# Optimization experiments

Hardware: AMD Instinct MI355X
Metric: run time of the kernel (lower is better)

## Reference

```python
import jax, jax.numpy as jnp
import numpy as np

D_MODEL = 256
D_INNER = 512   # expand * dim
D_STATE = 16
D_CONV = 4
DT_RANK = 16    # ceil(dim / 16)
PATCH = 64


def _silu(v):
    return v * jax.nn.sigmoid(v)


def _causal_dwconv(x, w, b):
    # x: (b, d, l); w: (d, 1, k) depthwise; causal left pad k-1
    y = jax.lax.conv_general_dilated(
        x, w, window_strides=(1,), padding=[(D_CONV - 1, 0)],
        feature_group_count=D_INNER, dimension_numbers=("NCH", "OIH", "NCH"))
    return y + b[None, :, None]


def _selective_scan(u, delta, A, Bm, Cm, Dp):
    # u, delta: (b, d, l); A: (d, n); Bm, Cm: (b, n, l)
    dA = jnp.exp(jnp.einsum("bdl,dn->lbdn", delta, A))
    dBu = jnp.einsum("bdl,bnl,bdl->lbdn", delta, Bm, u)
    Ct = jnp.transpose(Cm, (2, 0, 1))  # (l, b, n)

    def step(h, inp):
        dA_t, dBu_t, c_t = inp
        h = dA_t * h + dBu_t
        return h, jnp.einsum("bdn,bn->bd", h, c_t)

    h0 = jnp.zeros(u.shape[:2] + (A.shape[1],), u.dtype)
    _, ys = jax.lax.scan(step, h0, (dA, dBu, Ct))  # ys: (l, b, d)
    return jnp.transpose(ys, (1, 2, 0)) + Dp[None, :, None] * u


def _mamba_branch(xz, conv_w, conv_b, xproj_w, dtp_w, dtp_b, A_log, Dp):
    xpart, z = jnp.split(xz, 2, axis=1)  # each (b, d_inner, l)
    xc = _silu(_causal_dwconv(xpart, conv_w, conv_b))
    xdbl = jnp.einsum("bdl,ed->bel", xc, xproj_w)  # e = dt_rank + 2*d_state
    dt = xdbl[:, :DT_RANK]
    Bm = xdbl[:, DT_RANK:DT_RANK + D_STATE]
    Cm = xdbl[:, DT_RANK + D_STATE:]
    delta = jax.nn.softplus(jnp.einsum("brl,dr->bdl", dt, dtp_w) + dtp_b[None, :, None])
    A = -jnp.exp(A_log)
    y = _selective_scan(xc, delta, A, Bm, Cm, Dp)
    return y * _silu(z)


def setup_inputs():
    key = jax.random.key(0)
    ks = jax.random.split(key, 16)

    def nrm(k, shape, s=0.02):
        return jax.random.normal(k, shape, jnp.float32) * s

    A_init = jnp.log(jnp.tile(jnp.arange(1, D_STATE + 1, dtype=jnp.float32), (D_INNER, 1)))
    return {
        "x": jax.random.normal(ks[0], (2, D_MODEL, 4096), jnp.float32),
        "ln_g": jnp.ones((D_MODEL,), jnp.float32),
        "ln_b": jnp.zeros((D_MODEL,), jnp.float32),
        "in_proj_w": nrm(ks[1], (2 * D_INNER, D_MODEL)),
        "conv_w": nrm(ks[2], (D_INNER, 1, D_CONV), 0.1),
        "conv_b": nrm(ks[3], (D_INNER,), 0.01),
        "x_proj_w": nrm(ks[4], (DT_RANK + 2 * D_STATE, D_INNER)),
        "dt_proj_w": nrm(ks[5], (D_INNER, DT_RANK), 0.1),
        "dt_proj_b": nrm(ks[6], (D_INNER,), 0.1),
        "A_log": A_init,
        "D_f": jnp.ones((D_INNER,), jnp.float32),
        "conv_w_b": nrm(ks[7], (D_INNER, 1, D_CONV), 0.1),
        "conv_b_b": nrm(ks[8], (D_INNER,), 0.01),
        "x_proj_w_b": nrm(ks[9], (DT_RANK + 2 * D_STATE, D_INNER)),
        "dt_proj_w_b": nrm(ks[10], (D_INNER, DT_RANK), 0.1),
        "dt_proj_b_b": nrm(ks[11], (D_INNER,), 0.1),
        "A_b_log": A_init,
        "D_b": jnp.ones((D_INNER,), jnp.float32),
        "out_proj_w": nrm(ks[12], (D_MODEL, D_INNER)),
        "depth": 4,
    }


def reference(x, ln_g, ln_b, in_proj_w, conv_w, conv_b, x_proj_w, dt_proj_w,
              dt_proj_b, A_log, D_f, conv_w_b, conv_b_b, x_proj_w_b,
              dt_proj_w_b, dt_proj_b_b, A_b_log, D_b, out_proj_w, depth):
    assert depth in (3, 4, 5)
    B, C, L = x.shape
    ps = PATCH
    xp, Lp = x, L
    if L % ps != 0:  # borrow-pad (static shape logic, mirrors torch code)
        pad_len = ps - L % ps
        start = max(L - L % ps - pad_len, 0)
        xp = jnp.concatenate([x, x[:, :, start:start + pad_len]], axis=2)
        Lp = L + pad_len
    npt = Lp // ps
    # (B, C, npt, ps) -> (B*ps, C, npt) -> (B*ps, npt, C)
    xd = xp.reshape(B, C, npt, ps).transpose(0, 3, 1, 2).reshape(B * ps, C, npt)
    xf = jnp.transpose(xd, (0, 2, 1))
    # LayerNorm over channel dim
    mu = xf.mean(-1, keepdims=True)
    var = ((xf - mu) ** 2).mean(-1, keepdims=True)
    xn = (xf - mu) * jax.lax.rsqrt(var + 1e-5) * ln_g + ln_b
    # in_proj -> (b, 2*d_inner, l)
    xz = jnp.einsum("blc,ec->bel", xn, in_proj_w)
    y_f = _mamba_branch(xz, conv_w, conv_b, x_proj_w, dt_proj_w, dt_proj_b, A_log, D_f)
    y_b = _mamba_branch(xz[:, :, ::-1], conv_w_b, conv_b_b, x_proj_w_b,
                        dt_proj_w_b, dt_proj_b_b, A_b_log, D_b)[:, :, ::-1]
    y = y_f + y_b
    out_m = jnp.einsum("bdl,cd->blc", y, out_proj_w)  # (B*ps, npt, C)
    # mirrors torch: reshape(B, ps, npt, C).permute(0,3,1,2).reshape(B, C, Lp)
    xo = out_m.reshape(B, ps, npt, C).transpose(0, 3, 1, 2).reshape(B, C, Lp)
    xo = xo[:, :, :L]
    return xo + x
```

## Files before the change

kernel.cpp:

```cpp
#include <hip/hip_runtime.h>


#define OFF_XZ 0
#define OFF_XC 8388608
#define OFF_DL 12582912
#define OFF_BC 16777216
#define OFF_YF 17039360
#define OFF_YB 19136512
#define OFF_WOB 21233664
#define OFF_WX 21299200

typedef __attribute__((ext_vector_type(8))) short short8;
typedef __attribute__((ext_vector_type(4))) float f32x4;

__device__ __forceinline__ float siluf(float v) {
    return v / (1.f + __expf(-v));
}
__device__ __forceinline__ float softplusf(float v) {
    return (v > 20.f) ? v : log1pf(__expf(v));
}
__device__ __forceinline__ unsigned short f2bf(float f) {
    union { float f; unsigned int u; } v; v.f = f;
    unsigned int u = v.u;
    return (unsigned short)((u + 0x7FFFu + ((u >> 16) & 1u)) >> 16);
}

__global__ __launch_bounds__(256) void k_cvt_w(
    const float* __restrict__ W, unsigned short* __restrict__ Wb, int n4)
{
    int i = blockIdx.x * 256 + threadIdx.x;
    if (i >= n4) return;
    float4 v = *(const float4*)(W + i * 4);
    ushort4 o;
    o.x = f2bf(v.x); o.y = f2bf(v.y); o.z = f2bf(v.z); o.w = f2bf(v.w);
    *(ushort4*)(Wb + i * 4) = o;
}

__global__ __launch_bounds__(256) void k_mk_wx(
    const float* __restrict__ W6, const float* __restrict__ dtw,
    unsigned short* __restrict__ Wx)
{
    const int n = blockIdx.x;
    const int c = threadIdx.x;
    if (n < 512) {
        float a0 = 0.f, a1 = 0.f;
        #pragma unroll
        for (int r = 0; r < 16; ++r) {
            float w = dtw[n * 16 + r];
            a0 = fmaf(w, W6[r * 512 + c], a0);
            a1 = fmaf(w, W6[r * 512 + c + 256], a1);
        }
        Wx[n * 512 + c] = f2bf(a0);
        Wx[n * 512 + c + 256] = f2bf(a1);
    } else {
        int rr = n - 496;
        Wx[n * 512 + c] = f2bf(W6[rr * 512 + c]);
        Wx[n * 512 + c + 256] = f2bf(W6[rr * 512 + c + 256]);
    }
}

__global__ __launch_bounds__(256) void k_ln_inproj_mfma(
    const float* __restrict__ x, const float* __restrict__ g,
    const float* __restrict__ bt, const unsigned short* __restrict__ Wb,
    float* __restrict__ xz)
{
    __shared__ unsigned short sxb[64 * 256];
    const int bid = blockIdx.x;
    const int pg = bid >> 2, og = bid & 3;
    const int p0 = pg * 64;
    const int tid = threadIdx.x;
    const int wave = tid >> 6, lane = tid & 63;
    const int b = pg >> 6, pp = pg & 63;
    const float* xb = x + ((size_t)b * 256) * 4096 + pp;

    const int c = lane * 4;
    const float g0 = g[c + 0], g1 = g[c + 1], g2 = g[c + 2], g3 = g[c + 3];
    const float b0 = bt[c + 0], b1 = bt[c + 1], b2 = bt[c + 2], b3 = bt[c + 3];
    for (int i = 0; i < 16; ++i) {
        int m = wave * 16 + i;
        const float* xr = xb + m * 64;
        float v0 = xr[(size_t)(c + 0) * 4096];
        float v1 = xr[(size_t)(c + 1) * 4096];
        float v2 = xr[(size_t)(c + 2) * 4096];
        float v3 = xr[(size_t)(c + 3) * 4096];
        float s = v0 + v1 + v2 + v3;
        #pragma unroll
        for (int o = 32; o; o >>= 1) s += __shfl_xor(s, o);
        float mu = s * (1.f / 256.f);
        float q0 = v0 - mu, q1 = v1 - mu, q2 = v2 - mu, q3 = v3 - mu;
        float q = q0 * q0 + q1 * q1 + q2 * q2 + q3 * q3;
        #pragma unroll
        for (int o = 32; o; o >>= 1) q += __shfl_xor(q, o);
        float rs = rsqrtf(q * (1.f / 256.f) + 1e-5f);
        ushort4 pk;
        pk.x = f2bf(q0 * rs * g0 + b0);
        pk.y = f2bf(q1 * rs * g1 + b1);
        pk.z = f2bf(q2 * rs * g2 + b2);
        pk.w = f2bf(q3 * rs * g3 + b3);
        int byte = m * 512 + lane * 8;
        byte ^= (m & 7) << 4;
        *(ushort4*)((char*)sxb + byte) = pk;
    }
    __syncthreads();

    const int nbase = og * 256 + wave * 64;
    const int l15 = lane & 15, lg = lane >> 4;
    f32x4 acc[4][4];
    #pragma unroll
    for (int mi = 0; mi < 4; ++mi)
        #pragma unroll
        for (int ni = 0; ni < 4; ++ni) acc[mi][ni] = (f32x4){0.f, 0.f, 0.f, 0.f};

    const unsigned short* wrow[4];
    #pragma unroll
    for (int ni = 0; ni < 4; ++ni)
        wrow[ni] = Wb + (size_t)(nbase + ni * 16 + l15) * 256 + lg * 8;

    #pragma unroll 2
    for (int k0 = 0; k0 < 256; k0 += 32) {
        short8 a[4], bfr[4];
        #pragma unroll
        for (int mi = 0; mi < 4; ++mi) {
            int row = mi * 16 + l15;
            int byte = row * 512 + k0 * 2 + lg * 16;
            byte ^= (row & 7) << 4;
            a[mi] = *(const short8*)((const char*)sxb + byte);
        }
        #pragma unroll
        for (int ni = 0; ni < 4; ++ni)
            bfr[ni] = *(const short8*)(wrow[ni] + k0);
        #pragma unroll
        for (int mi = 0; mi < 4; ++mi)
            #pragma unroll
            for (int ni = 0; ni < 4; ++ni)
                acc[mi][ni] = __builtin_amdgcn_mfma_f32_16x16x32_bf16(
                    a[mi], bfr[ni], acc[mi][ni], 0, 0, 0);
    }

    #pragma unroll
    for (int mi = 0; mi < 4; ++mi)
        #pragma unroll
        for (int ni = 0; ni < 4; ++ni)
            #pragma unroll
            for (int r = 0; r < 4; ++r)
                xz[(size_t)(p0 + mi * 16 + lg * 4 + r) * 1024 + nbase + ni * 16 + l15] =
                    acc[mi][ni][r];
}

__global__ __launch_bounds__(256) void k_cxg(
    const float* __restrict__ xz, const float* __restrict__ cw,
    const float* __restrict__ cb, const unsigned short* __restrict__ Wx,
    const float* __restrict__ dtb,
    float* __restrict__ xc, float* __restrict__ delta,
    float* __restrict__ bcb, int rev)
{
    __shared__ unsigned short sxb[64 * 512];
    const int blk = blockIdx.x;
    const int bp = blk >> 1, og = blk & 1;
    const int tid = threadIdx.x;
    const int wave = tid >> 6, lane = tid & 63;
    const size_t xzrow = (size_t)bp * 64;
    const int m0 = wave * 16;

    {
        const int da = lane * 4, db = 256 + lane * 4;
        float4 wa0 = *(const float4*)&cw[(da + 0) * 4];
        float4 wa1 = *(const float4*)&cw[(da + 1) * 4];
        float4 wa2 = *(const float4*)&cw[(da + 2) * 4];
        float4 wa3 = *(const float4*)&cw[(da + 3) * 4];
        float4 wb0 = *(const float4*)&cw[(db + 0) * 4];
        float4 wb1 = *(const float4*)&cw[(db + 1) * 4];
        float4 wb2 = *(const float4*)&cw[(db + 2) * 4];
        float4 wb3 = *(const float4*)&cw[(db + 3) * 4];
        float4 ba = *(const float4*)&cb[da];
        float4 bb = *(const float4*)&cb[db];

        float4 a1 = {0,0,0,0}, a2 = {0,0,0,0}, a3 = {0,0,0,0};
        float4 c1 = {0,0,0,0}, c2 = {0,0,0,0}, c3 = {0,0,0,0};
        if (m0 > 0) {
            int i1 = m0 - 1, i2 = m0 - 2, i3 = m0 - 3;
            int l1 = rev ? 63 - i1 : i1, l2 = rev ? 63 - i2 : i2, l3 = rev ? 63 - i3 : i3;
            a1 = *(const float4*)&xz[(xzrow + l1) * 1024 + da];
            a2 = *(const float4*)&xz[(xzrow + l2) * 1024 + da];
            a3 = *(const float4*)&xz[(xzrow + l3) * 1024 + da];
            c1 = *(const float4*)&xz[(xzrow + l1) * 1024 + db];
            c2 = *(const float4*)&xz[(xzrow + l2) * 1024 + db];
            c3 = *(const float4*)&xz[(xzrow + l3) * 1024 + db];
        }
        for (int p = 0; p < 16; ++p) {
            int i = m0 + p;
            int l = rev ? 63 - i : i;
            float4 cura = *(const float4*)&xz[(xzrow + l) * 1024 + da];
            float4 curb = *(const float4*)&xz[(xzrow + l) * 1024 + db];
            float4 sa, sb;
            sa.x = siluf(wa0.w * cura.x + wa0.z * a1.x + wa0.y * a2.x + wa0.x * a3.x + ba.x);
            sa.y = siluf(wa1.w * cura.y + wa1.z * a1.y + wa1.y * a2.y + wa1.x * a3.y + ba.y);
            sa.z = siluf(wa2.w * cura.z + wa2.z * a1.z + wa2.y * a2.z + wa2.x * a3.z + ba.z);
            sa.w = siluf(wa3.w * cura.w + wa3.z * a1.w + wa3.y * a2.w + wa3.x * a3.w + ba.w);
            sb.x = siluf(wb0.w * curb.x + wb0.z * c1.x + wb0.y * c2.x + wb0.x * c3.x + bb.x);
            sb.y = siluf(wb1.w * curb.y + wb1.z * c1.y + wb1.y * c2.y + wb1.x * c3.y + bb.y);
            sb.z = siluf(wb2.w * curb.z + wb2.z * c1.z + wb2.y * c2.z + wb2.x * c3.z + bb.z);
            sb.w = siluf(wb3.w * curb.w + wb3.z * c1.w + wb3.y * c2.w + wb3.x * c3.w + bb.w);
            if (og == 0) {
                *(float4*)&xc[(xzrow + i) * 512 + da] = sa;
                *(float4*)&xc[(xzrow + i) * 512 + db] = sb;
            }
            ushort4 pa, pb;
            pa.x = f2bf(sa.x); pa.y = f2bf(sa.y); pa.z = f2bf(sa.z); pa.w = f2bf(sa.w);
            pb.x = f2bf(sb.x); pb.y = f2bf(sb.y); pb.z = f2bf(sb.z); pb.w = f2bf(sb.w);
            int bytea = i * 1024 + da * 2; bytea ^= (i & 7) << 4;
            int byteb = i * 1024 + db * 2; byteb ^= (i & 7) << 4;
            *(ushort4*)((char*)sxb + bytea) = pa;
            *(ushort4*)((char*)sxb + byteb) = pb;
            a3 = a2; a2 = a1; a1 = cura;
            c3 = c2; c2 = c1; c1 = curb;
        }
    }
    __syncthreads();

    const int l15 = lane & 15, lg = lane >> 4;
    f32x4 acc[17];
    #pragma unroll
    for (int ni = 0; ni < 17; ++ni) acc[ni] = (f32x4){0.f, 0.f, 0.f, 0.f};
    const unsigned short* bbase = Wx + (size_t)(og * 272 + l15) * 512 + lg * 8;
    const int arow = m0 + l15;
    const int abase = arow * 1024 + lg * 16;
    const int aswz = (arow & 7) << 4;

    for (int k0 = 0; k0 < 512; k0 += 32) {
        short8 af = *(const short8*)((const char*)sxb + ((abase + k0 * 2) ^ aswz));
        #pragma unroll
        for (int ni = 0; ni < 17; ++ni) {
            short8 bw = *(const short8*)(bbase + (size_t)ni * 8192 + k0);
            acc[ni] = __builtin_amdgcn_mfma_f32_16x16x32_bf16(af, bw, acc[ni], 0, 0, 0);
        }
    }

    #pragma unroll
    for (int ni = 0; ni < 17; ++ni) {
        int col = og * 272 + ni * 16 + l15;
        if (col < 512) {
            float bias = dtb[col];
            #pragma unroll
            for (int r = 0; r < 4; ++r) {
                int pos = m0 + lg * 4 + r;
                delta[(xzrow + pos) * 512 + col] = softplusf(acc[ni][r] + bias);
            }
        } else {
            #pragma unroll
            for (int r = 0; r < 4; ++r) {
                int pos = m0 + lg * 4 + r;
                bcb[(xzrow + pos) * 32 + (col - 512)] = acc[ni][r];
            }
        }
    }
}

__global__ __launch_bounds__(256) void k_scan(
    const float* __restrict__ delta, const float* __restrict__ u_,
    const float* __restrict__ bc_, const float* __restrict__ xz,
    const float* __restrict__ A_log, const float* __restrict__ Dp,
    unsigned short* __restrict__ yout, int rev)
{
    const int bid = blockIdx.x;
    const int bp  = bid >> 1;
    const int d   = ((bid & 1) << 8) + threadIdx.x;

    float a[16];
    #pragma unroll
    for (int n = 0; n < 16; ++n) a[n] = -__expf(A_log[(size_t)d * 16 + n]);
    const float Dd = Dp[d];

    float h[16];
    #pragma unroll
    for (int n = 0; n < 16; ++n) h[n] = 0.f;

    for (int l = 0; l < 64; ++l) {
        size_t base = (size_t)bp * 64 + l;
        float dl = delta[base * 512 + d];
        float uu = u_[base * 512 + d];
        float du = dl * uu;
        const float4* bc = (const float4*)(bc_ + base * 32);
        float y = 0.f;
        #pragma unroll
        for (int n4 = 0; n4 < 4; ++n4) {
            float4 Bv = bc[n4];
            float4 Cv = bc[4 + n4];
            int n = n4 * 4;
            h[n + 0] = fmaf(__expf(dl * a[n + 0]), h[n + 0], du * Bv.x); y = fmaf(h[n + 0], Cv.x, y);
            h[n + 1] = fmaf(__expf(dl * a[n + 1]), h[n + 1], du * Bv.y); y = fmaf(h[n + 1], Cv.y, y);
            h[n + 2] = fmaf(__expf(dl * a[n + 2]), h[n + 2], du * Bv.z); y = fmaf(h[n + 2], Cv.z, y);
            h[n + 3] = fmaf(__expf(dl * a[n + 3]), h[n + 3], du * Bv.w); y = fmaf(h[n + 3], Cv.w, y);
        }
        y = fmaf(Dd, uu, y);
        int lo = rev ? 63 - l : l;
        float zv = xz[((size_t)bp * 64 + lo) * 1024 + 512 + d];
        yout[((size_t)bp * 64 + lo) * 512 + d] = f2bf(y * siluf(zv));
    }
}

__global__ __launch_bounds__(256) void k_outproj_mfma(
    const unsigned short* __restrict__ yf, const unsigned short* __restrict__ yb,
    const unsigned short* __restrict__ wob, const float* __restrict__ x,
    float* __restrict__ out)
{
    __shared__ float sD[64][257];
    const int blk = blockIdx.x;
    const int g = blk >> 6, l = blk & 63;
    const int tid = threadIdx.x;
    const int wave = tid >> 6, lane = tid & 63;
    const int l15 = lane & 15, lg = lane >> 4;
    const int cbase = wave * 64;

    f32x4 acc[4][4];
    #pragma unroll
    for (int mi = 0; mi < 4; ++mi)
        #pragma unroll
        for (int ni = 0; ni < 4; ++ni) acc[mi][ni] = (f32x4){0.f, 0.f, 0.f, 0.f};

    const unsigned short* arf[4];
    const unsigned short* arb[4];
    #pragma unroll
    for (int mi = 0; mi < 4; ++mi) {
        size_t idx = (((size_t)(g * 64 + mi * 16 + l15)) * 64 + l) * 512 + lg * 8;
        arf[mi] = yf + idx;
        arb[mi] = yb + idx;
    }
    const unsigned short* brow[4];
    #pragma unroll
    for (int ni = 0; ni < 4; ++ni)
        brow[ni] = wob + (size_t)(cbase + ni * 16 + l15) * 512 + lg * 8;

    #pragma unroll 2
    for (int k0 = 0; k0 < 512; k0 += 32) {
        short8 bw[4], af[4], ab[4];
        #pragma unroll
        for (int ni = 0; ni < 4; ++ni) bw[ni] = *(const short8*)(brow[ni] + k0);
        #pragma unroll
        for (int mi = 0; mi < 4; ++mi) {
            af[mi] = *(const short8*)(arf[mi] + k0);
            ab[mi] = *(const short8*)(arb[mi] + k0);
        }
        #pragma unroll
        for (int mi = 0; mi < 4; ++mi)
            #pragma unroll
            for (int ni = 0; ni < 4; ++ni) {
                acc[mi][ni] = __builtin_amdgcn_mfma_f32_16x16x32_bf16(
                    af[mi], bw[ni], acc[mi][ni], 0, 0, 0);
                acc[mi][ni] = __builtin_amdgcn_mfma_f32_16x16x32_bf16(
                    ab[mi], bw[ni], acc[mi][ni], 0, 0, 0);
            }
    }

    #pragma unroll
    for (int mi = 0; mi < 4; ++mi)
        #pragma unroll
        for (int ni = 0; ni < 4; ++ni)
            #pragma unroll
            for (int r = 0; r < 4; ++r)
                sD[mi * 16 + lg * 4 + r][cbase + ni * 16 + l15] = acc[mi][ni][r];
    __syncthreads();

    #pragma unroll
    for (int q = 0; q < 16; ++q) {
        int f4 = q * 256 + tid;
        int cc = f4 >> 4, m4 = f4 & 15;
        size_t idx = ((size_t)(g * 256 + cc)) * 4096 + (size_t)l * 64 + m4 * 4;
        float4 xr = *(const float4*)(x + idx);
        float4 v;
        v.x = sD[m4 * 4 + 0][cc] + xr.x;
        v.y = sD[m4 * 4 + 1][cc] + xr.y;
        v.z = sD[m4 * 4 + 2][cc] + xr.z;
        v.w = sD[m4 * 4 + 3][cc] + xr.w;
        *(float4*)(out + idx) = v;
    }
}

extern "C" void kernel_launch(void* const* d_in, const int* in_sizes, int n_in,
                              void* d_out, int out_size, void* d_ws, size_t ws_size,
                              hipStream_t stream) {
    const float* x        = (const float*)d_in[0];
    const float* ln_g     = (const float*)d_in[1];
    const float* ln_b     = (const float*)d_in[2];
    const float* in_w     = (const float*)d_in[3];
    const float* conv_w   = (const float*)d_in[4];
    const float* conv_b   = (const float*)d_in[5];
    const float* xproj_w  = (const float*)d_in[6];
    const float* dtp_w    = (const float*)d_in[7];
    const float* dtp_b    = (const float*)d_in[8];
    const float* A_log    = (const float*)d_in[9];
    const float* D_f      = (const float*)d_in[10];
    const float* conv_w_b = (const float*)d_in[11];
    const float* conv_b_b = (const float*)d_in[12];
    const float* xproj_wb = (const float*)d_in[13];
    const float* dtp_w_b  = (const float*)d_in[14];
    const float* dtp_b_b  = (const float*)d_in[15];
    const float* A_b_log  = (const float*)d_in[16];
    const float* D_b      = (const float*)d_in[17];
    const float* out_w    = (const float*)d_in[18];
    float* out = (float*)d_out;

    float* ws  = (float*)d_ws;
    float* xz  = ws + OFF_XZ;
    float* xc  = ws + OFF_XC;
    float* dl  = ws + OFF_DL;
    float* bc  = ws + OFF_BC;
    unsigned short* w_bf = (unsigned short*)(ws + OFF_BC);
    unsigned short* yf   = (unsigned short*)(ws + OFF_YF);
    unsigned short* yb   = (unsigned short*)(ws + OFF_YB);
    unsigned short* wob  = (unsigned short*)(ws + OFF_WOB);
    unsigned short* wx   = (unsigned short*)(ws + OFF_WX);

    k_cvt_w<<<256, 256, 0, stream>>>(in_w, w_bf, 65536);
    k_cvt_w<<<128, 256, 0, stream>>>(out_w, wob, 32768);
    k_ln_inproj_mfma<<<512, 256, 0, stream>>>(x, ln_g, ln_b, w_bf, xz);
    k_mk_wx<<<544, 256, 0, stream>>>(xproj_w, dtp_w, wx);
    k_cxg<<<256, 256, 0, stream>>>(xz, conv_w, conv_b, wx, dtp_b, xc, dl, bc, 0);
    k_scan<<<256, 256, 0, stream>>>(dl, xc, bc, xz, A_log, D_f, yf, 0);
    k_mk_wx<<<544, 256, 0, stream>>>(xproj_wb, dtp_w_b, wx);
    k_cxg<<<256, 256, 0, stream>>>(xz, conv_w_b, conv_b_b, wx, dtp_b_b, xc, dl, bc, 1);
    k_scan<<<256, 256, 0, stream>>>(dl, xc, bc, xz, A_b_log, D_b, yb, 1);
    k_outproj_mfma<<<128, 256, 0, stream>>>(yf, yb, wob, x, out);
}
```

Before: 394.5 us.

## Merge weight-prep kernels and split conv/x_proj blocks by position quarter

Folds the two bf16 weight conversions and both x_proj/dt_proj weight builds into a single prep launch. The fused weights are written into the yf/yb buffers, which stay unused until the scans write them. The conv+x_proj kernel now uses 512 blocks, each owning 16 sequence positions and all 544 output columns spread across the 4 waves. This removes the duplicated depthwise conv + SiLU work that the two column-half blocks used to repeat, and shrinks shared memory per block. In exchange each block re-reads its 3-position conv halo, and the waves get an uneven 9/9/8/8 split of output tiles.

Result: faster. 366.6 us (-7.1%).

```diff
diff --git a/kernel.cpp b/kernel.cpp
--- a/kernel.cpp
+++ b/kernel.cpp
@@ -8,7 +8,6 @@
 #define OFF_YF 17039360
 #define OFF_YB 19136512
 #define OFF_WOB 21233664
-#define OFF_WX 21299200
 
 typedef __attribute__((ext_vector_type(8))) short short8;
 typedef __attribute__((ext_vector_type(4))) float f32x4;
@@ -25,23 +24,10 @@
     return (unsigned short)((u + 0x7FFFu + ((u >> 16) & 1u)) >> 16);
 }
 
-__global__ __launch_bounds__(256) void k_cvt_w(
-    const float* __restrict__ W, unsigned short* __restrict__ Wb, int n4)
-{
-    int i = blockIdx.x * 256 + threadIdx.x;
-    if (i >= n4) return;
-    float4 v = *(const float4*)(W + i * 4);
-    ushort4 o;
-    o.x = f2bf(v.x); o.y = f2bf(v.y); o.z = f2bf(v.z); o.w = f2bf(v.w);
-    *(ushort4*)(Wb + i * 4) = o;
-}
-
-__global__ __launch_bounds__(256) void k_mk_wx(
+__device__ __forceinline__ void mk_wx_row(
     const float* __restrict__ W6, const float* __restrict__ dtw,
-    unsigned short* __restrict__ Wx)
-{
-    const int n = blockIdx.x;
-    const int c = threadIdx.x;
+    unsigned short* __restrict__ Wx, int n, int c)
+{
     if (n < 512) {
         float a0 = 0.f, a1 = 0.f;
         #pragma unroll
@@ -56,6 +42,33 @@
         int rr = n - 496;
         Wx[n * 512 + c] = f2bf(W6[rr * 512 + c]);
         Wx[n * 512 + c + 256] = f2bf(W6[rr * 512 + c + 256]);
+    }
+}
+
+__global__ __launch_bounds__(256) void k_prep(
+    const float* __restrict__ in_w, const float* __restrict__ out_w,
+    const float* __restrict__ W6f, const float* __restrict__ dtwf,
+    const float* __restrict__ W6b, const float* __restrict__ dtwb,
+    unsigned short* __restrict__ w_bf, unsigned short* __restrict__ wob,
+    unsigned short* __restrict__ wxf, unsigned short* __restrict__ wxb)
+{
+    const int bid = blockIdx.x, t = threadIdx.x;
+    if (bid < 256) {
+        int i = (bid * 256 + t) * 4;
+        float4 v = *(const float4*)(in_w + i);
+        ushort4 o;
+        o.x = f2bf(v.x); o.y = f2bf(v.y); o.z = f2bf(v.z); o.w = f2bf(v.w);
+        *(ushort4*)(w_bf + i) = o;
+    } else if (bid < 384) {
+        int i = ((bid - 256) * 256 + t) * 4;
+        float4 v = *(const float4*)(out_w + i);
+        ushort4 o;
+        o.x = f2bf(v.x); o.y = f2bf(v.y); o.z = f2bf(v.z); o.w = f2bf(v.w);
+        *(ushort4*)(wob + i) = o;
+    } else if (bid < 928) {
+        mk_wx_row(W6f, dtwf, wxf, bid - 384, t);
+    } else {
+        mk_wx_row(W6b, dtwb, wxb, bid - 928, t);
     }
 }
 
@@ -154,103 +167,77 @@
     float* __restrict__ xc, float* __restrict__ delta,
     float* __restrict__ bcb, int rev)
 {
-    __shared__ unsigned short sxb[64 * 512];
+    __shared__ unsigned short sxb[16 * 512];
     const int blk = blockIdx.x;
-    const int bp = blk >> 1, og = blk & 1;
+    const int bp = blk >> 2, mq = blk & 3;
+    const int i0 = mq << 4;
     const int tid = threadIdx.x;
     const int wave = tid >> 6, lane = tid & 63;
     const size_t xzrow = (size_t)bp * 64;
-    const int m0 = wave * 16;
 
     {
-        const int da = lane * 4, db = 256 + lane * 4;
-        float4 wa0 = *(const float4*)&cw[(da + 0) * 4];
-        float4 wa1 = *(const float4*)&cw[(da + 1) * 4];
-        float4 wa2 = *(const float4*)&cw[(da + 2) * 4];
-        float4 wa3 = *(const float4*)&cw[(da + 3) * 4];
-        float4 wb0 = *(const float4*)&cw[(db + 0) * 4];
-        float4 wb1 = *(const float4*)&cw[(db + 1) * 4];
-        float4 wb2 = *(const float4*)&cw[(db + 2) * 4];
-        float4 wb3 = *(const float4*)&cw[(db + 3) * 4];
-        float4 ba = *(const float4*)&cb[da];
-        float4 bb = *(const float4*)&cb[db];
-
-        float4 a1 = {0,0,0,0}, a2 = {0,0,0,0}, a3 = {0,0,0,0};
-        float4 c1 = {0,0,0,0}, c2 = {0,0,0,0}, c3 = {0,0,0,0};
-        if (m0 > 0) {
-            int i1 = m0 - 1, i2 = m0 - 2, i3 = m0 - 3;
-            int l1 = rev ? 63 - i1 : i1, l2 = rev ? 63 - i2 : i2, l3 = rev ? 63 - i3 : i3;
-            a1 = *(const float4*)&xz[(xzrow + l1) * 1024 + da];
-            a2 = *(const float4*)&xz[(xzrow + l2) * 1024 + da];
-            a3 = *(const float4*)&xz[(xzrow + l3) * 1024 + da];
-            c1 = *(const float4*)&xz[(xzrow + l1) * 1024 + db];
-            c2 = *(const float4*)&xz[(xzrow + l2) * 1024 + db];
-            c3 = *(const float4*)&xz[(xzrow + l3) * 1024 + db];
+        const int c0 = tid * 2;
+        float4 w0 = *(const float4*)&cw[c0 * 4];
+        float4 w1 = *(const float4*)&cw[(c0 + 1) * 4];
+        float2 bb = *(const float2*)&cb[c0];
+        float2 h1 = {0.f, 0.f}, h2 = {0.f, 0.f}, h3 = {0.f, 0.f};
+        if (i0 > 0) {
+            h1 = *(const float2*)&xz[(xzrow + (rev ? 63 - (i0 - 1) : i0 - 1)) * 1024 + c0];
+            h2 = *(const float2*)&xz[(xzrow + (rev ? 63 - (i0 - 2) : i0 - 2)) * 1024 + c0];
+            h3 = *(const float2*)&xz[(xzrow + (rev ? 63 - (i0 - 3) : i0 - 3)) * 1024 + c0];
         }
         for (int p = 0; p < 16; ++p) {
-            int i = m0 + p;
+            int i = i0 + p;
             int l = rev ? 63 - i : i;
-            float4 cura = *(const float4*)&xz[(xzrow + l) * 1024 + da];
-            float4 curb = *(const float4*)&xz[(xzrow + l) * 1024 + db];
-            float4 sa, sb;
-            sa.x = siluf(wa0.w * cura.x + wa0.z * a1.x + wa0.y * a2.x + wa0.x * a3.x + ba.x);
-            sa.y = siluf(wa1.w * cura.y + wa1.z * a1.y + wa1.y * a2.y + wa1.x * a3.y + ba.y);
-            sa.z = siluf(wa2.w * cura.z + wa2.z * a1.z + wa2.y * a2.z + wa2.x * a3.z + ba.z);
-            sa.w = siluf(wa3.w * cura.w + wa3.z * a1.w + wa3.y * a2.w + wa3.x * a3.w + ba.w);
-            sb.x = siluf(wb0.w * curb.x + wb0.z * c1.x + wb0.y * c2.x + wb0.x * c3.x + bb.x);
-            sb.y = siluf(wb1.w * curb.y + wb1.z * c1.y + wb1.y * c2.y + wb1.x * c3.y + bb.y);
-            sb.z = siluf(wb2.w * curb.z + wb2.z * c1.z + wb2.y * c2.z + wb2.x * c3.z + bb.z);
-            sb.w = siluf(wb3.w * curb.w + wb3.z * c1.w + wb3.y * c2.w + wb3.x * c3.w + bb.w);
-            if (og == 0) {
-                *(float4*)&xc[(xzrow + i) * 512 + da] = sa;
-                *(float4*)&xc[(xzrow + i) * 512 + db] = sb;
-            }
-            ushort4 pa, pb;
-            pa.x = f2bf(sa.x); pa.y = f2bf(sa.y); pa.z = f2bf(sa.z); pa.w = f2bf(sa.w);
-            pb.x = f2bf(sb.x); pb.y = f2bf(sb.y); pb.z = f2bf(sb.z); pb.w = f2bf(sb.w);
-            int bytea = i * 1024 + da * 2; bytea ^= (i & 7) << 4;
-            int byteb = i * 1024 + db * 2; byteb ^= (i & 7) << 4;
-            *(ushort4*)((char*)sxb + bytea) = pa;
-            *(ushort4*)((char*)sxb + byteb) = pb;
-            a3 = a2; a2 = a1; a1 = cura;
-            c3 = c2; c2 = c1; c1 = curb;
+            float2 cur = *(const float2*)&xz[(xzrow + l) * 1024 + c0];
+            float s0 = siluf(w0.w * cur.x + w0.z * h1.x + w0.y * h2.x + w0.x * h3.x + bb.x);
+            float s1 = siluf(w1.w * cur.y + w1.z * h1.y + w1.y * h2.y + w1.x * h3.y + bb.y);
+            float2 sv; sv.x = s0; sv.y = s1;
+            *(float2*)&xc[(xzrow + i) * 512 + c0] = sv;
+            int byte = p * 1024 + c0 * 2;
+            byte ^= (p & 7) << 4;
+            ushort2 pk; pk.x = f2bf(s0); pk.y = f2bf(s1);
+            *(ushort2*)((char*)sxb + byte) = pk;
+            h3 = h2; h2 = h1; h1 = cur;
         }
     }
     __syncthreads();
 
     const int l15 = lane & 15, lg = lane >> 4;
-    f32x4 acc[17];
-    #pragma unroll
-    for (int ni = 0; ni < 17; ++ni) acc[ni] = (f32x4){0.f, 0.f, 0.f, 0.f};
-    const unsigned short* bbase = Wx + (size_t)(og * 272 + l15) * 512 + lg * 8;
-    const int arow = m0 + l15;
-    const int abase = arow * 1024 + lg * 16;
-    const int aswz = (arow & 7) << 4;
+    const int nt = (wave < 2) ? 9 : 8;
+    const int tbase = (wave < 2) ? wave * 9 : 18 + (wave - 2) * 8;
+    f32x4 acc[9];
+    #pragma unroll
+    for (int ni = 0; ni < 9; ++ni) acc[ni] = (f32x4){0.f, 0.f, 0.f, 0.f};
+    const unsigned short* bbase = Wx + (size_t)(tbase * 16 + l15) * 512 + lg * 8;
+    const int abase = l15 * 1024 + lg * 16;
+    const int aswz = (l15 & 7) << 4;
 
     for (int k0 = 0; k0 < 512; k0 += 32) {
         short8 af = *(const short8*)((const char*)sxb + ((abase + k0 * 2) ^ aswz));
         #pragma unroll
-        for (int ni = 0; ni < 17; ++ni) {
-            short8 bw = *(const short8*)(bbase + (size_t)ni * 8192 + k0);
-            acc[ni] = __builtin_amdgcn_mfma_f32_16x16x32_bf16(af, bw, acc[ni], 0, 0, 0);
-        }
-    }
-
-    #pragma unroll
-    for (int ni = 0; ni < 17; ++ni) {
-        int col = og * 272 + ni * 16 + l15;
-        if (col < 512) {
-            float bias = dtb[col];
-            #pragma unroll
-            for (int r = 0; r < 4; ++r) {
-                int pos = m0 + lg * 4 + r;
-                delta[(xzrow + pos) * 512 + col] = softplusf(acc[ni][r] + bias);
+        for (int ni = 0; ni < 9; ++ni) {
+            if (ni < nt) {
+                short8 bw = *(const short8*)(bbase + (size_t)ni * 8192 + k0);
+                acc[ni] = __builtin_amdgcn_mfma_f32_16x16x32_bf16(af, bw, acc[ni], 0, 0, 0);
             }
-        } else {
-            #pragma unroll
-            for (int r = 0; r < 4; ++r) {
-                int pos = m0 + lg * 4 + r;
-                bcb[(xzrow + pos) * 32 + (col - 512)] = acc[ni][r];
+        }
+    }
+
+    #pragma unroll
+    for (int ni = 0; ni < 9; ++ni) {
+        if (ni < nt) {
+            int col = (tbase + ni) * 16 + l15;
+            if (col < 512) {
+                float bias = dtb[col];
+                #pragma unroll
+                for (int r = 0; r < 4; ++r)
+                    delta[(xzrow + i0 + lg * 4 + r) * 512 + col] =
+                        softplusf(acc[ni][r] + bias);
+            } else {
+                #pragma unroll
+                for (int r = 0; r < 4; ++r)
+                    bcb[(xzrow + i0 + lg * 4 + r) * 32 + (col - 512)] = acc[ni][r];
             }
         }
     }
@@ -409,16 +396,15 @@
     unsigned short* yf   = (unsigned short*)(ws + OFF_YF);
     unsigned short* yb   = (unsigned short*)(ws + OFF_YB);
     unsigned short* wob  = (unsigned short*)(ws + OFF_WOB);
-    unsigned short* wx   = (unsigned short*)(ws + OFF_WX);
-
-    k_cvt_w<<<256, 256, 0, stream>>>(in_w, w_bf, 65536);
-    k_cvt_w<<<128, 256, 0, stream>>>(out_w, wob, 32768);
+    unsigned short* wxf  = yf;
+    unsigned short* wxb  = yb;
+
+    k_prep<<<1472, 256, 0, stream>>>(in_w, out_w, xproj_w, dtp_w, xproj_wb, dtp_w_b,
+                                     w_bf, wob, wxf, wxb);
     k_ln_inproj_mfma<<<512, 256, 0, stream>>>(x, ln_g, ln_b, w_bf, xz);
-    k_mk_wx<<<544, 256, 0, stream>>>(xproj_w, dtp_w, wx);
-    k_cxg<<<256, 256, 0, stream>>>(xz, conv_w, conv_b, wx, dtp_b, xc, dl, bc, 0);
+    k_cxg<<<512, 256, 0, stream>>>(xz, conv_w, conv_b, wxf, dtp_b, xc, dl, bc, 0);
     k_scan<<<256, 256, 0, stream>>>(dl, xc, bc, xz, A_log, D_f, yf, 0);
-    k_mk_wx<<<544, 256, 0, stream>>>(xproj_wb, dtp_w_b, wx);
-    k_cxg<<<256, 256, 0, stream>>>(xz, conv_w_b, conv_b_b, wx, dtp_b_b, xc, dl, bc, 1);
+    k_cxg<<<512, 256, 0, stream>>>(xz, conv_w_b, conv_b_b, wxb, dtp_b_b, xc, dl, bc, 1);
     k_scan<<<256, 256, 0, stream>>>(dl, xc, bc, xz, A_b_log, D_b, yb, 1);
     k_outproj_mfma<<<128, 256, 0, stream>>>(yf, yb, wob, x, out);
 }
```

## Store intermediates in bf16 and run both scan branches in single merged launches

Applied to the files above, without the earlier changes.

The xz, xc and delta intermediates are now stored as bf16 instead of fp32, which roughly halves global memory traffic between kernels. The forward and backward branches are merged into single conv/x-proj and scan launches of 512 blocks each, using separate per-branch buffers, so the two directions run concurrently with more blocks in flight. All weight conversions are folded into one prep kernel that reuses the output buffers as scratch. This costs extra rounding on the activations, which changes accuracy relative to the fp32 path.

New measurement: 323.3 us. 18.0% less time.

```diff
diff --git a/kernel.cpp b/kernel.cpp
--- a/kernel.cpp
+++ b/kernel.cpp
@@ -1,14 +1,16 @@
 #include <hip/hip_runtime.h>
 
 
-#define OFF_XZ 0
-#define OFF_XC 8388608
-#define OFF_DL 12582912
-#define OFF_BC 16777216
-#define OFF_YF 17039360
-#define OFF_YB 19136512
-#define OFF_WOB 21233664
-#define OFF_WX 21299200
+#define OFF_XZ   0
+#define OFF_XCF  4194304
+#define OFF_XCB  6291456
+#define OFF_DLF  8388608
+#define OFF_DLB  10485760
+#define OFF_BCF  12582912
+#define OFF_BCB  12845056
+#define OFF_YF   13107200
+#define OFF_YB   15204352
+#define OFF_WOB  17301504
 
 typedef __attribute__((ext_vector_type(8))) short short8;
 typedef __attribute__((ext_vector_type(4))) float f32x4;
@@ -24,24 +26,19 @@
     unsigned int u = v.u;
     return (unsigned short)((u + 0x7FFFu + ((u >> 16) & 1u)) >> 16);
 }
-
-__global__ __launch_bounds__(256) void k_cvt_w(
-    const float* __restrict__ W, unsigned short* __restrict__ Wb, int n4)
-{
-    int i = blockIdx.x * 256 + threadIdx.x;
-    if (i >= n4) return;
-    float4 v = *(const float4*)(W + i * 4);
-    ushort4 o;
-    o.x = f2bf(v.x); o.y = f2bf(v.y); o.z = f2bf(v.z); o.w = f2bf(v.w);
-    *(ushort4*)(Wb + i * 4) = o;
-}
-
-__global__ __launch_bounds__(256) void k_mk_wx(
+__device__ __forceinline__ float bf2f(unsigned short u) {
+    union { unsigned int u; float f; } v; v.u = ((unsigned int)u) << 16;
+    return v.f;
+}
+__device__ __forceinline__ float4 bf4(ushort4 u) {
+    float4 f; f.x = bf2f(u.x); f.y = bf2f(u.y); f.z = bf2f(u.z); f.w = bf2f(u.w);
+    return f;
+}
+
+__device__ __forceinline__ void mk_wx_row(
     const float* __restrict__ W6, const float* __restrict__ dtw,
-    unsigned short* __restrict__ Wx)
-{
-    const int n = blockIdx.x;
-    const int c = threadIdx.x;
+    unsigned short* __restrict__ Wx, int n, int c)
+{
     if (n < 512) {
         float a0 = 0.f, a1 = 0.f;
         #pragma unroll
@@ -59,10 +56,37 @@
     }
 }
 
+__global__ __launch_bounds__(256) void k_prep(
+    const float* __restrict__ in_w, const float* __restrict__ out_w,
+    const float* __restrict__ W6f, const float* __restrict__ dtwf,
+    const float* __restrict__ W6b, const float* __restrict__ dtwb,
+    unsigned short* __restrict__ w_bf, unsigned short* __restrict__ wob,
+    unsigned short* __restrict__ wxf, unsigned short* __restrict__ wxb)
+{
+    const int bid = blockIdx.x, t = threadIdx.x;
+    if (bid < 256) {
+        int i = (bid * 256 + t) * 4;
+        float4 v = *(const float4*)(in_w + i);
+        ushort4 o;
+        o.x = f2bf(v.x); o.y = f2bf(v.y); o.z = f2bf(v.z); o.w = f2bf(v.w);
+        *(ushort4*)(w_bf + i) = o;
+    } else if (bid < 384) {
+        int i = ((bid - 256) * 256 + t) * 4;
+        float4 v = *(const float4*)(out_w + i);
+        ushort4 o;
+        o.x = f2bf(v.x); o.y = f2bf(v.y); o.z = f2bf(v.z); o.w = f2bf(v.w);
+        *(ushort4*)(wob + i) = o;
+    } else if (bid < 928) {
+        mk_wx_row(W6f, dtwf, wxf, bid - 384, t);
+    } else {
+        mk_wx_row(W6b, dtwb, wxb, bid - 928, t);
+    }
+}
+
 __global__ __launch_bounds__(256) void k_ln_inproj_mfma(
     const float* __restrict__ x, const float* __restrict__ g,
     const float* __restrict__ bt, const unsigned short* __restrict__ Wb,
-    float* __restrict__ xz)
+    unsigned short* __restrict__ xz)
 {
     __shared__ unsigned short sxb[64 * 256];
     const int bid = blockIdx.x;
@@ -144,19 +168,34 @@
             #pragma unroll
             for (int r = 0; r < 4; ++r)
                 xz[(size_t)(p0 + mi * 16 + lg * 4 + r) * 1024 + nbase + ni * 16 + l15] =
-                    acc[mi][ni][r];
-}
-
-__global__ __launch_bounds__(256) void k_cxg(
-    const float* __restrict__ xz, const float* __restrict__ cw,
-    const float* __restrict__ cb, const unsigned short* __restrict__ Wx,
-    const float* __restrict__ dtb,
-    float* __restrict__ xc, float* __restrict__ delta,
-    float* __restrict__ bcb, int rev)
+                    f2bf(acc[mi][ni][r]);
+}
+
+__global__ __launch_bounds__(256) void k_cxg2(
+    const unsigned short* __restrict__ xz,
+    const float* __restrict__ cwf, const float* __restrict__ cbf,
+    const unsigned short* __restrict__ wxf, const float* __restrict__ dtbf,
+    const float* __restrict__ cwb, const float* __restrict__ cbb,
+    const unsigned short* __restrict__ wxb, const float* __restrict__ dtbb,
+    unsigned short* __restrict__ xcf, unsigned short* __restrict__ dlf,
+    float* __restrict__ bcf,
+    unsigned short* __restrict__ xcb, unsigned short* __restrict__ dlb,
+    float* __restrict__ bcb_)
 {
     __shared__ unsigned short sxb[64 * 512];
-    const int blk = blockIdx.x;
-    const int bp = blk >> 1, og = blk & 1;
+    const int bid = blockIdx.x;
+    const int branch = bid >> 8;
+    const int rr = bid & 255;
+    const int bp = rr >> 1, og = rr & 1;
+    const int rev = branch;
+    const float* cw = branch ? cwb : cwf;
+    const float* cb = branch ? cbb : cbf;
+    const unsigned short* Wx = branch ? wxb : wxf;
+    const float* dtb = branch ? dtbb : dtbf;
+    unsigned short* xc = branch ? xcb : xcf;
+    unsigned short* delta = branch ? dlb : dlf;
+    float* bcb = branch ? bcb_ : bcf;
+
     const int tid = threadIdx.x;
     const int wave = tid >> 6, lane = tid & 63;
     const size_t xzrow = (size_t)bp * 64;
@@ -180,34 +219,31 @@
         if (m0 > 0) {
             int i1 = m0 - 1, i2 = m0 - 2, i3 = m0 - 3;
             int l1 = rev ? 63 - i1 : i1, l2 = rev ? 63 - i2 : i2, l3 = rev ? 63 - i3 : i3;
-            a1 = *(const float4*)&xz[(xzrow + l1) * 1024 + da];
-            a2 = *(const float4*)&xz[(xzrow + l2) * 1024 + da];
-            a3 = *(const float4*)&xz[(xzrow + l3) * 1024 + da];
-            c1 = *(const float4*)&xz[(xzrow + l1) * 1024 + db];
-            c2 = *(const float4*)&xz[(xzrow + l2) * 1024 + db];
-            c3 = *(const float4*)&xz[(xzrow + l3) * 1024 + db];
+            a1 = bf4(*(const ushort4*)&xz[(xzrow + l1) * 1024 + da]);
+            a2 = bf4(*(const ushort4*)&xz[(xzrow + l2) * 1024 + da]);
+            a3 = bf4(*(const ushort4*)&xz[(xzrow + l3) * 1024 + da]);
+            c1 = bf4(*(const ushort4*)&xz[(xzrow + l1) * 1024 + db]);
+            c2 = bf4(*(const ushort4*)&xz[(xzrow + l2) * 1024 + db]);
+            c3 = bf4(*(const ushort4*)&xz[(xzrow + l3) * 1024 + db]);
         }
         for (int p = 0; p < 16; ++p) {
             int i = m0 + p;
             int l = rev ? 63 - i : i;
-            float4 cura = *(const float4*)&xz[(xzrow + l) * 1024 + da];
-            float4 curb = *(const float4*)&xz[(xzrow + l) * 1024 + db];
-            float4 sa, sb;
-            sa.x = siluf(wa0.w * cura.x + wa0.z * a1.x + wa0.y * a2.x + wa0.x * a3.x + ba.x);
-            sa.y = siluf(wa1.w * cura.y + wa1.z * a1.y + wa1.y * a2.y + wa1.x * a3.y + ba.y);
-            sa.z = siluf(wa2.w * cura.z + wa2.z * a1.z + wa2.y * a2.z + wa2.x * a3.z + ba.z);
-            sa.w = siluf(wa3.w * cura.w + wa3.z * a1.w + wa3.y * a2.w + wa3.x * a3.w + ba.w);
-            sb.x = siluf(wb0.w * curb.x + wb0.z * c1.x + wb0.y * c2.x + wb0.x * c3.x + bb.x);
-            sb.y = siluf(wb1.w * curb.y + wb1.z * c1.y + wb1.y * c2.y + wb1.x * c3.y + bb.y);
-            sb.z = siluf(wb2.w * curb.z + wb2.z * c1.z + wb2.y * c2.z + wb2.x * c3.z + bb.z);
-            sb.w = siluf(wb3.w * curb.w + wb3.z * c1.w + wb3.y * c2.w + wb3.x * c3.w + bb.w);
+            float4 cura = bf4(*(const ushort4*)&xz[(xzrow + l) * 1024 + da]);
+            float4 curb = bf4(*(const ushort4*)&xz[(xzrow + l) * 1024 + db]);
+            ushort4 pa, pb;
+            pa.x = f2bf(siluf(wa0.w * cura.x + wa0.z * a1.x + wa0.y * a2.x + wa0.x * a3.x + ba.x));
+            pa.y = f2bf(siluf(wa1.w * cura.y + wa1.z * a1.y + wa1.y * a2.y + wa1.x * a3.y + ba.y));
+            pa.z = f2bf(siluf(wa2.w * cura.z + wa2.z * a1.z + wa2.y * a2.z + wa2.x * a3.z + ba.z));
+            pa.w = f2bf(siluf(wa3.w * cura.w + wa3.z * a1.w + wa3.y * a2.w + wa3.x * a3.w + ba.w));
+            pb.x = f2bf(siluf(wb0.w * curb.x + wb0.z * c1.x + wb0.y * c2.x + wb0.x * c3.x + bb.x));
+            pb.y = f2bf(siluf(wb1.w * curb.y + wb1.z * c1.y + wb1.y * c2.y + wb1.x * c3.y + bb.y));
+            pb.z = f2bf(siluf(wb2.w * curb.z + wb2.z * c1.z + wb2.y * c2.z + wb2.x * c3.z + bb.z));
+            pb.w = f2bf(siluf(wb3.w * curb.w + wb3.z * c1.w + wb3.y * c2.w + wb3.x * c3.w + bb.w));
             if (og == 0) {
-                *(float4*)&xc[(xzrow + i) * 512 + da] = sa;
-                *(float4*)&xc[(xzrow + i) * 512 + db] = sb;
+                *(ushort4*)&xc[(xzrow + i) * 512 + da] = pa;
+                *(ushort4*)&xc[(xzrow + i) * 512 + db] = pb;
             }
-            ushort4 pa, pb;
-            pa.x = f2bf(sa.x); pa.y = f2bf(sa.y); pa.z = f2bf(sa.z); pa.w = f2bf(sa.w);
-            pb.x = f2bf(sb.x); pb.y = f2bf(sb.y); pb.z = f2bf(sb.z); pb.w = f2bf(sb.w);
             int bytea = i * 1024 + da * 2; bytea ^= (i & 7) << 4;
             int byteb = i * 1024 + db * 2; byteb ^= (i & 7) << 4;
             *(ushort4*)((char*)sxb + bytea) = pa;
@@ -244,7 +280,7 @@
             #pragma unroll
             for (int r = 0; r < 4; ++r) {
                 int pos = m0 + lg * 4 + r;
-                delta[(xzrow + pos) * 512 + col] = softplusf(acc[ni][r] + bias);
+                delta[(xzrow + pos) * 512 + col] = f2bf(softplusf(acc[ni][r] + bias));
             }
         } else {
             #pragma unroll
@@ -256,15 +292,28 @@
     }
 }
 
-__global__ __launch_bounds__(256) void k_scan(
-    const float* __restrict__ delta, const float* __restrict__ u_,
-    const float* __restrict__ bc_, const float* __restrict__ xz,
-    const float* __restrict__ A_log, const float* __restrict__ Dp,
-    unsigned short* __restrict__ yout, int rev)
+__global__ __launch_bounds__(256) void k_scan2(
+    const unsigned short* __restrict__ dlf, const unsigned short* __restrict__ xcf,
+    const float* __restrict__ bcf,
+    const unsigned short* __restrict__ dlb, const unsigned short* __restrict__ xcb,
+    const float* __restrict__ bcb_,
+    const unsigned short* __restrict__ xz,
+    const float* __restrict__ A_logf, const float* __restrict__ Dpf,
+    const float* __restrict__ A_logb, const float* __restrict__ Dpb,
+    unsigned short* __restrict__ yf, unsigned short* __restrict__ yb)
 {
     const int bid = blockIdx.x;
-    const int bp  = bid >> 1;
-    const int d   = ((bid & 1) << 8) + threadIdx.x;
+    const int branch = bid >> 8;
+    const int rr = bid & 255;
+    const int bp  = rr >> 1;
+    const int d   = ((rr & 1) << 8) + threadIdx.x;
+    const unsigned short* delta = branch ? dlb : dlf;
+    const unsigned short* u_ = branch ? xcb : xcf;
+    const float* bc_ = branch ? bcb_ : bcf;
+    const float* A_log = branch ? A_logb : A_logf;
+    const float* Dp = branch ? Dpb : Dpf;
+    unsigned short* yout = branch ? yb : yf;
+    const int rev = branch;
 
     float a[16];
     #pragma unroll
@@ -277,8 +326,8 @@
 
     for (int l = 0; l < 64; ++l) {
         size_t base = (size_t)bp * 64 + l;
-        float dl = delta[base * 512 + d];
-        float uu = u_[base * 512 + d];
+        float dl = bf2f(delta[base * 512 + d]);
+        float uu = bf2f(u_[base * 512 + d]);
         float du = dl * uu;
         const float4* bc = (const float4*)(bc_ + base * 32);
         float y = 0.f;
@@ -294,7 +343,7 @@
         }
         y = fmaf(Dd, uu, y);
         int lo = rev ? 63 - l : l;
-        float zv = xz[((size_t)bp * 64 + lo) * 1024 + 512 + d];
+        float zv = bf2f(xz[((size_t)bp * 64 + lo) * 1024 + 512 + d]);
         yout[((size_t)bp * 64 + lo) * 512 + d] = f2bf(y * siluf(zv));
     }
 }
@@ -401,24 +450,27 @@
     float* out = (float*)d_out;
 
     float* ws  = (float*)d_ws;
-    float* xz  = ws + OFF_XZ;
-    float* xc  = ws + OFF_XC;
-    float* dl  = ws + OFF_DL;
-    float* bc  = ws + OFF_BC;
-    unsigned short* w_bf = (unsigned short*)(ws + OFF_BC);
-    unsigned short* yf   = (unsigned short*)(ws + OFF_YF);
-    unsigned short* yb   = (unsigned short*)(ws + OFF_YB);
-    unsigned short* wob  = (unsigned short*)(ws + OFF_WOB);
-    unsigned short* wx   = (unsigned short*)(ws + OFF_WX);
-
-    k_cvt_w<<<256, 256, 0, stream>>>(in_w, w_bf, 65536);
-    k_cvt_w<<<128, 256, 0, stream>>>(out_w, wob, 32768);
-    k_ln_inproj_mfma<<<512, 256, 0, stream>>>(x, ln_g, ln_b, w_bf, xz);
-    k_mk_wx<<<544, 256, 0, stream>>>(xproj_w, dtp_w, wx);
-    k_cxg<<<256, 256, 0, stream>>>(xz, conv_w, conv_b, wx, dtp_b, xc, dl, bc, 0);
-    k_scan<<<256, 256, 0, stream>>>(dl, xc, bc, xz, A_log, D_f, yf, 0);
-    k_mk_wx<<<544, 256, 0, stream>>>(xproj_wb, dtp_w_b, wx);
-    k_cxg<<<256, 256, 0, stream>>>(xz, conv_w_b, conv_b_b, wx, dtp_b_b, xc, dl, bc, 1);
-    k_scan<<<256, 256, 0, stream>>>(dl, xc, bc, xz, A_b_log, D_b, yb, 1);
+    unsigned short* xzb = (unsigned short*)(ws + OFF_XZ);
+    unsigned short* xcf = (unsigned short*)(ws + OFF_XCF);
+    unsigned short* xcb = (unsigned short*)(ws + OFF_XCB);
+    unsigned short* dlf = (unsigned short*)(ws + OFF_DLF);
+    unsigned short* dlb = (unsigned short*)(ws + OFF_DLB);
+    float* bcf = ws + OFF_BCF;
+    float* bcb = ws + OFF_BCB;
+    unsigned short* w_bf = (unsigned short*)(ws + OFF_BCF);
+    unsigned short* yf  = (unsigned short*)(ws + OFF_YF);
+    unsigned short* yb  = (unsigned short*)(ws + OFF_YB);
+    unsigned short* wob = (unsigned short*)(ws + OFF_WOB);
+    unsigned short* wxf = yf;
+    unsigned short* wxb = yb;
+
+    k_prep<<<1472, 256, 0, stream>>>(in_w, out_w, xproj_w, dtp_w, xproj_wb, dtp_w_b,
+                                     w_bf, wob, wxf, wxb);
+    k_ln_inproj_mfma<<<512, 256, 0, stream>>>(x, ln_g, ln_b, w_bf, xzb);
+    k_cxg2<<<512, 256, 0, stream>>>(xzb, conv_w, conv_b, wxf, dtp_b,
+                                    conv_w_b, conv_b_b, wxb, dtp_b_b,
+                                    xcf, dlf, bcf, xcb, dlb, bcb);
+    k_scan2<<<512, 256, 0, stream>>>(dlf, xcf, bcf, dlb, xcb, bcb, xzb,
+                                     A_log, D_f, A_b_log, D_b, yf, yb);
     k_outproj_mfma<<<128, 256, 0, stream>>>(yf, yb, wob, x, out);
 }
```
